# Kernel tuning notes

Hardware: AMD Instinct MI355X
Metric: run time of the kernel (lower is better)

The kernel has to match this reference:

```python
import jax, jax.numpy as jnp
import numpy as np

SEQ, BATCH, C_P, C, C_I = 192, 2, 128, 32, 128


def setup_inputs() -> dict:
    key = jax.random.key(0)
    ks = jax.random.split(key, 9)
    s = lambda k, shape, scale: jax.random.normal(k, shape, dtype=jnp.float32) * scale
    return {
        "p": s(ks[0], (SEQ, BATCH, C_P), 1.0),
        "gamma": jnp.ones((C_P,), jnp.float32) + s(ks[1], (C_P,), 0.02),
        "beta": s(ks[2], (C_P,), 0.02),
        "W1": s(ks[3], (C, C_P), 1.0 / np.sqrt(C_P)),
        "b1": s(ks[4], (C,), 0.02),
        "W2": s(ks[5], (C, C_P), 1.0 / np.sqrt(C_P)),
        "b2": s(ks[6], (C,), 0.02),
        "Wout": s(ks[7], (C_I, C * C), 1.0 / np.sqrt(C * C)),
        "bout": s(ks[8], (C_I,), 0.02),
    }


def reference(p, gamma, beta, W1, b1, W2, b2, Wout, bout):
    eps = 1e-5
    B = p.shape[-2]  # Batch = p.size(-2)
    # LayerNorm over c_p
    mu = jnp.mean(p, axis=-1, keepdims=True)
    var = jnp.var(p, axis=-1, keepdims=True)
    pn = (p - mu) * jax.lax.rsqrt(var + eps) * gamma + beta
    # dual linear projections, then permute (seq, batch, c) -> (batch, seq, c)
    p1 = jnp.einsum('sbp,cp->bsc', pn, W1) + b1
    p2 = jnp.einsum('sbp,cp->bsc', pn, W2) + b2
    # outer product + flatten(c,d) + linear_out, reassociated as a single contraction:
    # out[b,k,i,j] = sum_{c,d} p1[b,i,c] * p2[b,j,d] * Wout[k, c*C+d]
    Wk = Wout.reshape(Wout.shape[0], p1.shape[-1], p2.shape[-1])  # (c_i, c, c)
    out = jnp.einsum('bic,bjd,kcd->bkij', p1, p2, Wk)
    out = (out + bout[None, :, None, None]) / B  # bias is also divided, as in source
    return out  # (batch, c_i, seq, seq)
```

## Files before the change

kernel.cpp:

```cpp
#include <hip/hip_runtime.h>
#include <hip/hip_bf16.h>


#define SEQ 192
#define BATCH 2
#define CP 128
#define CDIM 32
#define CI 128

typedef __attribute__((ext_vector_type(8))) short bf16x8;
typedef __attribute__((ext_vector_type(4))) float f32x4;

static __device__ __forceinline__ short f2bf(float f) {
    unsigned u = __builtin_bit_cast(unsigned, f);
    u += 0x7fffu + ((u >> 16) & 1u);
    return (short)(u >> 16);
}

__global__ __launch_bounds__(128) void opm_pre(
    const float* __restrict__ p, const float* __restrict__ gamma,
    const float* __restrict__ beta, const float* __restrict__ W1,
    const float* __restrict__ b1, const float* __restrict__ W2,
    const float* __restrict__ b2,
    short* __restrict__ p1ws, short* __restrict__ p2ws)
{
    int row = blockIdx.x;
    int s = row >> 1, b = row & 1;
    int t = threadIdx.x;

    __shared__ float pns[CP];
    __shared__ float red[4];
    __shared__ float part[CP];

    float x = p[s * (BATCH * CP) + b * CP + t];
    float s1 = x, s2 = x * x;
    #pragma unroll
    for (int off = 32; off; off >>= 1) {
        s1 += __shfl_down(s1, off);
        s2 += __shfl_down(s2, off);
    }
    int wave = t >> 6, lane = t & 63;
    if (lane == 0) { red[wave * 2] = s1; red[wave * 2 + 1] = s2; }
    __syncthreads();
    float tot  = red[0] + red[2];
    float tot2 = red[1] + red[3];
    float mu  = tot * (1.0f / CP);
    float var = tot2 * (1.0f / CP) - mu * mu;
    float rs  = rsqrtf(var + 1e-5f);
    pns[t] = (x - mu) * rs * gamma[t] + beta[t];
    __syncthreads();

    int c = t & 63, half = t >> 6;
    const float* wrow = (c < CDIM ? W1 + c * CP : W2 + (c - CDIM) * CP) + half * 64;
    const float4* pn4 = (const float4*)(pns + half * 64);
    const float4* w4p = (const float4*)wrow;
    float acc = 0.0f;
    #pragma unroll
    for (int i = 0; i < 16; ++i) {
        float4 w4 = w4p[i];
        float4 pn = pn4[i];
        acc += w4.x * pn.x + w4.y * pn.y + w4.z * pn.z + w4.w * pn.w;
    }
    part[t] = acc;
    __syncthreads();
    if (t < 64) {
        float d = part[t] + part[t + 64];
        if (c < CDIM) {
            p1ws[(b * SEQ + s) * CDIM + c] = f2bf(d + b1[c]);
        } else {
            p2ws[(b * SEQ + s) * CDIM + (c - CDIM)] =
                f2bf(0.5f * (d + b2[c - CDIM]));
        }
    }
}

#define T2PAD 40

__global__ __launch_bounds__(256) void opm_main(
    const short* __restrict__ p1ws,
    const short* __restrict__ p2ws,
    const float* __restrict__ Wout,
    const float* __restrict__ bout,
    float* __restrict__ out)
{
    int bk = blockIdx.x >> 2;
    int iq = blockIdx.x & 3;
    int b = bk >> 7, k = bk & 127;
    int tid  = threadIdx.x;
    int wave = tid >> 6, lane = tid & 63;
    int l15  = lane & 15, quad = lane >> 4;

    __shared__ short t2s[SEQ * T2PAD];

    const float* wk = Wout + k * (CDIM * CDIM);
    bf16x8 bfr[2];
    #pragma unroll
    for (int ni = 0; ni < 2; ++ni) {
        const float* wrow = wk + (ni * 16 + l15) * CDIM + quad * 8;
        #pragma unroll
        for (int e = 0; e < 8; ++e) bfr[ni][e] = f2bf(wrow[e]);
    }
    #pragma unroll
    for (int mi = 0; mi < 3; ++mi) {
        int j0 = (wave * 3 + mi) * 16;
        bf16x8 afrag = *(const bf16x8*)(p2ws + (b * SEQ + j0 + l15) * CDIM + quad * 8);
        #pragma unroll
        for (int ni = 0; ni < 2; ++ni) {
            f32x4 acc = {0.0f, 0.0f, 0.0f, 0.0f};
            acc = __builtin_amdgcn_mfma_f32_16x16x32_bf16(afrag, bfr[ni], acc, 0, 0, 0);
            #pragma unroll
            for (int r = 0; r < 4; ++r)
                t2s[(j0 + quad * 4 + r) * T2PAD + ni * 16 + l15] = f2bf(acc[r]);
        }
    }

    float biask = 0.5f * bout[k];
    const short* p1b = p1ws + b * SEQ * CDIM;
    float* obase = out + (size_t)bk * (SEQ * SEQ);
    #pragma unroll
    for (int ii = 0; ii < 3; ++ii) {
        int i0 = iq * 48 + ii * 16;
        bf16x8 afrag = *(const bf16x8*)(p1b + (i0 + l15) * CDIM + quad * 8);
        #pragma unroll
        for (int jj = 0; jj < 3; ++jj) {
            int j0 = (wave * 3 + jj) * 16;
            bf16x8 bfrag = *(const bf16x8*)(t2s + (j0 + l15) * T2PAD + quad * 8);
            f32x4 acc = {biask, biask, biask, biask};
            acc = __builtin_amdgcn_mfma_f32_16x16x32_bf16(afrag, bfrag, acc, 0, 0, 0);
            float* o = obase + (i0 + quad * 4) * SEQ + j0 + l15;
            #pragma unroll
            for (int r = 0; r < 4; ++r)
                o[r * SEQ] = acc[r];
        }
    }
}

extern "C" void kernel_launch(void* const* d_in, const int* in_sizes, int n_in,
                              void* d_out, int out_size, void* d_ws, size_t ws_size,
                              hipStream_t stream) {
    const float* p     = (const float*)d_in[0];
    const float* gamma = (const float*)d_in[1];
    const float* beta  = (const float*)d_in[2];
    const float* W1    = (const float*)d_in[3];
    const float* b1    = (const float*)d_in[4];
    const float* W2    = (const float*)d_in[5];
    const float* b2    = (const float*)d_in[6];
    const float* Wout  = (const float*)d_in[7];
    const float* bout  = (const float*)d_in[8];
    float* out = (float*)d_out;

    short* p1ws = (short*)d_ws;
    short* p2ws = p1ws + BATCH * SEQ * CDIM;

    opm_pre<<<SEQ * BATCH, 128, 0, stream>>>(p, gamma, beta, W1, b1, W2, b2,
                                             p1ws, p2ws);
    opm_main<<<BATCH * CI * 4, 256, 0, stream>>>(p1ws, p2ws, Wout, bout, out);
}
```

Before: 88.78 us.

## Fuse LayerNorm and projections into main kernel, recomputing per block

```diff
diff --git a/kernel.cpp b/kernel.cpp
--- a/kernel.cpp
+++ b/kernel.cpp
@@ -7,6 +7,7 @@
 #define CP 128
 #define CDIM 32
 #define CI 128
+#define PAD 40
 
 typedef __attribute__((ext_vector_type(8))) short bf16x8;
 typedef __attribute__((ext_vector_type(4))) float f32x4;
@@ -17,71 +18,12 @@
     return (short)(u >> 16);
 }
 
-__global__ __launch_bounds__(128) void opm_pre(
+__global__ __launch_bounds__(256, 4) void opm_fused(
     const float* __restrict__ p, const float* __restrict__ gamma,
     const float* __restrict__ beta, const float* __restrict__ W1,
     const float* __restrict__ b1, const float* __restrict__ W2,
-    const float* __restrict__ b2,
-    short* __restrict__ p1ws, short* __restrict__ p2ws)
-{
-    int row = blockIdx.x;
-    int s = row >> 1, b = row & 1;
-    int t = threadIdx.x;
-
-    __shared__ float pns[CP];
-    __shared__ float red[4];
-    __shared__ float part[CP];
-
-    float x = p[s * (BATCH * CP) + b * CP + t];
-    float s1 = x, s2 = x * x;
-    #pragma unroll
-    for (int off = 32; off; off >>= 1) {
-        s1 += __shfl_down(s1, off);
-        s2 += __shfl_down(s2, off);
-    }
-    int wave = t >> 6, lane = t & 63;
-    if (lane == 0) { red[wave * 2] = s1; red[wave * 2 + 1] = s2; }
-    __syncthreads();
-    float tot  = red[0] + red[2];
-    float tot2 = red[1] + red[3];
-    float mu  = tot * (1.0f / CP);
-    float var = tot2 * (1.0f / CP) - mu * mu;
-    float rs  = rsqrtf(var + 1e-5f);
-    pns[t] = (x - mu) * rs * gamma[t] + beta[t];
-    __syncthreads();
-
-    int c = t & 63, half = t >> 6;
-    const float* wrow = (c < CDIM ? W1 + c * CP : W2 + (c - CDIM) * CP) + half * 64;
-    const float4* pn4 = (const float4*)(pns + half * 64);
-    const float4* w4p = (const float4*)wrow;
-    float acc = 0.0f;
-    #pragma unroll
-    for (int i = 0; i < 16; ++i) {
-        float4 w4 = w4p[i];
-        float4 pn = pn4[i];
-        acc += w4.x * pn.x + w4.y * pn.y + w4.z * pn.z + w4.w * pn.w;
-    }
-    part[t] = acc;
-    __syncthreads();
-    if (t < 64) {
-        float d = part[t] + part[t + 64];
-        if (c < CDIM) {
-            p1ws[(b * SEQ + s) * CDIM + c] = f2bf(d + b1[c]);
-        } else {
-            p2ws[(b * SEQ + s) * CDIM + (c - CDIM)] =
-                f2bf(0.5f * (d + b2[c - CDIM]));
-        }
-    }
-}
-
-#define T2PAD 40
-
-__global__ __launch_bounds__(256) void opm_main(
-    const short* __restrict__ p1ws,
-    const short* __restrict__ p2ws,
-    const float* __restrict__ Wout,
-    const float* __restrict__ bout,
-    float* __restrict__ out)
+    const float* __restrict__ b2, const float* __restrict__ Wout,
+    const float* __restrict__ bout, float* __restrict__ out)
 {
     int bk = blockIdx.x >> 2;
     int iq = blockIdx.x & 3;
@@ -90,7 +32,107 @@
     int wave = tid >> 6, lane = tid & 63;
     int l15  = lane & 15, quad = lane >> 4;
 
-    __shared__ short t2s[SEQ * T2PAD];
+    __shared__ float mu_s[SEQ];
+    __shared__ float rs_s[SEQ];
+    __shared__ short slab[SEQ * PAD];
+    __shared__ short p2s[SEQ * PAD];
+    __shared__ short p1s[48 * PAD];
+
+    if (tid < SEQ) {
+        const float4* pr = (const float4*)(p + tid * (BATCH * CP) + b * CP);
+        float s1 = 0.0f, s2 = 0.0f;
+        #pragma unroll
+        for (int i = 0; i < CP / 4; ++i) {
+            float4 v = pr[i];
+            s1 += v.x + v.y + v.z + v.w;
+            s2 += v.x * v.x + v.y * v.y + v.z * v.z + v.w * v.w;
+        }
+        float mu  = s1 * (1.0f / CP);
+        float var = s2 * (1.0f / CP) - mu * mu;
+        mu_s[tid] = mu;
+        rs_s[tid] = rsqrtf(var + 1e-5f);
+    }
+    __syncthreads();
+
+    bool doP1 = (wave == iq);
+    f32x4 accP2[3][2], accP1[3][2];
+    #pragma unroll
+    for (int mi = 0; mi < 3; ++mi)
+        #pragma unroll
+        for (int nt = 0; nt < 2; ++nt) {
+            float v2 = 0.5f * b2[nt * 16 + l15];
+            float v1 = b1[nt * 16 + l15];
+            accP2[mi][nt] = (f32x4){v2, v2, v2, v2};
+            accP1[mi][nt] = (f32x4){v1, v1, v1, v1};
+        }
+
+    int r0 = tid >> 3, c4 = (tid & 7) * 4;
+    for (int kt = 0; kt < 4; ++kt) {
+        float4 g4  = *(const float4*)(gamma + kt * 32 + c4);
+        float4 be4 = *(const float4*)(beta  + kt * 32 + c4);
+        #pragma unroll
+        for (int pp = 0; pp < 6; ++pp) {
+            int row = pp * 32 + r0;
+            float4 v = *(const float4*)(p + row * (BATCH * CP) + b * CP + kt * 32 + c4);
+            float mu = mu_s[row], rs = rs_s[row];
+            short4 o;
+            o.x = f2bf((v.x - mu) * rs * g4.x + be4.x);
+            o.y = f2bf((v.y - mu) * rs * g4.y + be4.y);
+            o.z = f2bf((v.z - mu) * rs * g4.z + be4.z);
+            o.w = f2bf((v.w - mu) * rs * g4.w + be4.w);
+            *(short4*)(slab + row * PAD + c4) = o;
+        }
+        __syncthreads();
+
+        #pragma unroll
+        for (int mi = 0; mi < 3; ++mi) {
+            int i0 = (wave * 3 + mi) * 16;
+            bf16x8 af = *(const bf16x8*)(slab + (i0 + l15) * PAD + quad * 8);
+            #pragma unroll
+            for (int nt = 0; nt < 2; ++nt) {
+                const float* w = W2 + (nt * 16 + l15) * CP + kt * 32 + quad * 8;
+                bf16x8 bf;
+                #pragma unroll
+                for (int e = 0; e < 8; ++e) bf[e] = f2bf(0.5f * w[e]);
+                accP2[mi][nt] = __builtin_amdgcn_mfma_f32_16x16x32_bf16(
+                    af, bf, accP2[mi][nt], 0, 0, 0);
+            }
+            if (doP1) {
+                #pragma unroll
+                for (int nt = 0; nt < 2; ++nt) {
+                    const float* w = W1 + (nt * 16 + l15) * CP + kt * 32 + quad * 8;
+                    bf16x8 bf;
+                    #pragma unroll
+                    for (int e = 0; e < 8; ++e) bf[e] = f2bf(w[e]);
+                    accP1[mi][nt] = __builtin_amdgcn_mfma_f32_16x16x32_bf16(
+                        af, bf, accP1[mi][nt], 0, 0, 0);
+                }
+            }
+        }
+        __syncthreads();
+    }
+
+    #pragma unroll
+    for (int mi = 0; mi < 3; ++mi) {
+        int i0 = (wave * 3 + mi) * 16;
+        #pragma unroll
+        for (int nt = 0; nt < 2; ++nt)
+            #pragma unroll
+            for (int r = 0; r < 4; ++r)
+                p2s[(i0 + quad * 4 + r) * PAD + nt * 16 + l15] =
+                    f2bf(accP2[mi][nt][r]);
+    }
+    if (doP1) {
+        #pragma unroll
+        for (int mi = 0; mi < 3; ++mi)
+            #pragma unroll
+            for (int nt = 0; nt < 2; ++nt)
+                #pragma unroll
+                for (int r = 0; r < 4; ++r)
+                    p1s[(mi * 16 + quad * 4 + r) * PAD + nt * 16 + l15] =
+                        f2bf(accP1[mi][nt][r]);
+    }
+    __syncthreads();
 
     const float* wk = Wout + k * (CDIM * CDIM);
     bf16x8 bfr[2];
@@ -103,30 +145,29 @@
     #pragma unroll
     for (int mi = 0; mi < 3; ++mi) {
         int j0 = (wave * 3 + mi) * 16;
-        bf16x8 afrag = *(const bf16x8*)(p2ws + (b * SEQ + j0 + l15) * CDIM + quad * 8);
+        bf16x8 af = *(const bf16x8*)(p2s + (j0 + l15) * PAD + quad * 8);
         #pragma unroll
         for (int ni = 0; ni < 2; ++ni) {
             f32x4 acc = {0.0f, 0.0f, 0.0f, 0.0f};
-            acc = __builtin_amdgcn_mfma_f32_16x16x32_bf16(afrag, bfr[ni], acc, 0, 0, 0);
+            acc = __builtin_amdgcn_mfma_f32_16x16x32_bf16(af, bfr[ni], acc, 0, 0, 0);
             #pragma unroll
             for (int r = 0; r < 4; ++r)
-                t2s[(j0 + quad * 4 + r) * T2PAD + ni * 16 + l15] = f2bf(acc[r]);
+                slab[(j0 + quad * 4 + r) * PAD + ni * 16 + l15] = f2bf(acc[r]);
         }
     }
 
     float biask = 0.5f * bout[k];
-    const short* p1b = p1ws + b * SEQ * CDIM;
     float* obase = out + (size_t)bk * (SEQ * SEQ);
     #pragma unroll
     for (int ii = 0; ii < 3; ++ii) {
         int i0 = iq * 48 + ii * 16;
-        bf16x8 afrag = *(const bf16x8*)(p1b + (i0 + l15) * CDIM + quad * 8);
+        bf16x8 af = *(const bf16x8*)(p1s + (ii * 16 + l15) * PAD + quad * 8);
         #pragma unroll
         for (int jj = 0; jj < 3; ++jj) {
             int j0 = (wave * 3 + jj) * 16;
-            bf16x8 bfrag = *(const bf16x8*)(t2s + (j0 + l15) * T2PAD + quad * 8);
+            bf16x8 bf = *(const bf16x8*)(slab + (j0 + l15) * PAD + quad * 8);
             f32x4 acc = {biask, biask, biask, biask};
-            acc = __builtin_amdgcn_mfma_f32_16x16x32_bf16(afrag, bfrag, acc, 0, 0, 0);
+            acc = __builtin_amdgcn_mfma_f32_16x16x32_bf16(af, bf, acc, 0, 0, 0);
             float* o = obase + (i0 + quad * 4) * SEQ + j0 + l15;
             #pragma unroll
             for (int r = 0; r < 4; ++r)
@@ -149,10 +190,6 @@
     const float* bout  = (const float*)d_in[8];
     float* out = (float*)d_out;
 
-    short* p1ws = (short*)d_ws;
-    short* p2ws = p1ws + BATCH * SEQ * CDIM;
-
-    opm_pre<<<SEQ * BATCH, 128, 0, stream>>>(p, gamma, beta, W1, b1, W2, b2,
-                                             p1ws, p2ws);
-    opm_main<<<BATCH * CI * 4, 256, 0, stream>>>(p1ws, p2ws, Wout, bout, out);
+    opm_fused<<<BATCH * CI * 4, 256, 0, stream>>>(
+        p, gamma, beta, W1, b1, W2, b2, Wout, bout, out);
 }
```

Measured after the change: 115.0 us. 1.3x slower.
